# Performance work log

Measured on AMD Instinct MI355X. Metric: run time of the kernel, lower is better.

## Reference

```python
import jax, jax.numpy as jnp
import numpy as np

# ---- MMAL-Net canonical configuration (baked constants of the module) ----
STRIDE = 32          # backbone stride: feature cell -> input pixels
FM = 14              # feature-map side (448 / 32)
RATIOS = [[4, 4], [3, 5], [5, 3],
          [6, 6], [5, 7], [7, 5],
          [8, 8], [6, 10], [10, 6], [7, 9], [9, 7]]
GROUP_SLICES = [(0, 3), (3, 6), (6, 11)]   # 3 scale groups of ratios
N_LIST = [3, 2, 1]                          # proposals kept per group
IOU_THRESHS = [0.25, 0.25, 0.25]


def _make_coords():
    # pixel-space [x0, y0, x1, y1] per sliding window, row-major (i outer, j inner)
    # matching the row-major flatten of the pooled feature maps.
    c = []
    for rh, rw in RATIOS:
        for i in range(FM - rh + 1):
            for j in range(FM - rw + 1):
                c.append([j * STRIDE, i * STRIDE,
                          (j + rw) * STRIDE - 1, (i + rh) * STRIDE - 1])
    return jnp.asarray(np.array(c, np.float32))

COORDS = _make_coords()                                   # [837, 4]
WIN_NUMS = [(FM - rh + 1) * (FM - rw + 1) for rh, rw in RATIOS]
GROUP_WINS = [sum(WIN_NUMS[a:b]) for a, b in GROUP_SLICES]  # [361, 241, 235]
GROUP_OFFSETS = [0, GROUP_WINS[0], GROUP_WINS[0] + GROUP_WINS[1]]
TOTAL_WINS = sum(GROUP_WINS)                              # 837


def _window_scores(x):
    """sum_c avgpool(x, r) == avgpool(sum_c x, r) -- fuse the channel reduction
    first so we avoid materializing [B, C, h', w'] per ratio."""
    y = jnp.sum(x, axis=1)  # [B, H, W]
    parts = []
    for rh, rw in RATIOS:
        s = jax.lax.reduce_window(y, jnp.float32(0), jax.lax.add,
                                  (1, rh, rw), (1, 1, 1), 'VALID') / (rh * rw)
        parts.append(s.reshape(y.shape[0], -1))
    return jnp.concatenate(parts, axis=1)  # [B, TOTAL_WINS]


def _nms_group(scores, coords, n_sel, iou_thresh):
    """Greedy NMS on one scale group: fixed n_sel iterations of
    (argmax over surviving windows, suppress IoU > thresh). If candidates run
    out, the last selected index is repeated (matches the torch fallback)."""
    W = scores.shape[0]
    area = (coords[:, 2] - coords[:, 0] + 1.) * (coords[:, 3] - coords[:, 1] + 1.)

    def step(carry, _):
        valid, last = carry
        any_v = jnp.any(valid)
        idx = jnp.argmax(jnp.where(valid, scores, -jnp.inf))
        idx = jnp.where(any_v, idx, last)
        sel = coords[idx]
        lt = jnp.maximum(coords[:, :2], sel[:2])
        rb = jnp.minimum(coords[:, 2:], sel[2:])
        wh = rb - lt + 1.
        inter = jnp.where((wh[:, 0] < 0) | (wh[:, 1] < 0), 0., wh[:, 0] * wh[:, 1])
        iou = inter / (area + area[idx] - inter)
        new_valid = (valid & (iou <= iou_thresh)).at[idx].set(False)
        new_valid = jnp.where(any_v, new_valid, valid)
        return (new_valid, idx), idx

    (_, _), sel = jax.lax.scan(step, (jnp.ones(W, bool), jnp.int32(0)),
                               None, length=n_sel)
    return sel  # [n_sel] int32 local indices


def setup_inputs() -> dict:
    key = jax.random.key(0)
    x = jax.random.normal(key, (64, 2048, FM, FM), dtype=jnp.float32)
    return {"x": x, "proposalN": 6}


def reference(x, proposalN):
    all_scores = _window_scores(x)  # [B, 837]
    idx_parts = []
    for g in range(len(N_LIST)):
        off, W = GROUP_OFFSETS[g], GROUP_WINS[g]
        sc = all_scores[:, off:off + W]
        co = COORDS[off:off + W]
        sel = jax.vmap(lambda s: _nms_group(s, co, N_LIST[g], IOU_THRESHS[g]))(sc)
        idx_parts.append(sel + off)
    proposal_indices = jnp.concatenate(idx_parts, axis=1)  # [B, proposalN]
    proposal_scores = jnp.take_along_axis(all_scores, proposal_indices, axis=1)
    return proposal_indices, proposal_scores, all_scores
```

## Files before the change

kernel.cpp:

```cpp
#include <hip/hip_runtime.h>
#include <math.h>

#define B 64
#define C 2048
#define FMH 14
#define HW 196
#define HW4 49
#define CHUNKS 32
#define CPC (C / CHUNKS)
#define NWIN 837
#define KMAX 6

__device__ __constant__ int d_RH[11]   = {4, 3, 5, 6, 5, 7, 8, 6, 10, 7, 9};
__device__ __constant__ int d_RW[11]   = {4, 5, 3, 6, 7, 5, 8, 10, 6, 9, 7};
__device__ __constant__ int d_WOFF[12] = {0, 121, 241, 361, 442, 522, 602, 651, 696, 741, 789, 837};

__global__ __launch_bounds__(256) void sum_channels_kernel(const float4* __restrict__ x,
                                                           float4* __restrict__ partial) {
    const int chunk = blockIdx.x;
    const int b     = blockIdx.y;
    const int lane  = threadIdx.x & 63;
    const int wave  = threadIdx.x >> 6;

    float4 a0 = make_float4(0.f, 0.f, 0.f, 0.f);
    float4 a1 = a0, a2 = a0, a3 = a0;
    if (lane < HW4) {
        const float4* base = x + (size_t)(b * C + chunk * CPC) * HW4 + lane;
        #pragma unroll
        for (int k = 0; k < CPC / 4; k += 4) {
            float4 v0 = base[(size_t)(wave + 4 * (k + 0)) * HW4];
            float4 v1 = base[(size_t)(wave + 4 * (k + 1)) * HW4];
            float4 v2 = base[(size_t)(wave + 4 * (k + 2)) * HW4];
            float4 v3 = base[(size_t)(wave + 4 * (k + 3)) * HW4];
            a0.x += v0.x; a0.y += v0.y; a0.z += v0.z; a0.w += v0.w;
            a1.x += v1.x; a1.y += v1.y; a1.z += v1.z; a1.w += v1.w;
            a2.x += v2.x; a2.y += v2.y; a2.z += v2.z; a2.w += v2.w;
            a3.x += v3.x; a3.y += v3.y; a3.z += v3.z; a3.w += v3.w;
        }
    }
    float4 acc;
    acc.x = (a0.x + a1.x) + (a2.x + a3.x);
    acc.y = (a0.y + a1.y) + (a2.y + a3.y);
    acc.z = (a0.z + a1.z) + (a2.z + a3.z);
    acc.w = (a0.w + a1.w) + (a2.w + a3.w);

    __shared__ float4 sh[256];
    sh[threadIdx.x] = acc;
    __syncthreads();

    if (threadIdx.x < 64 && lane < HW4) {
        float4 c0 = sh[lane], c1 = sh[64 + lane], c2 = sh[128 + lane], c3 = sh[192 + lane];
        float4 s;
        s.x = (c0.x + c1.x) + (c2.x + c3.x);
        s.y = (c0.y + c1.y) + (c2.y + c3.y);
        s.z = (c0.z + c1.z) + (c2.z + c3.z);
        s.w = (c0.w + c1.w) + (c2.w + c3.w);
        partial[(size_t)(b * CHUNKS + chunk) * HW4 + lane] = s;
    }
}

__device__ inline void decode_box(int w, float& x0, float& y0, float& x1, float& y1, float& area) {
    int r = 0;
    while (w >= d_WOFF[r + 1]) ++r;
    int local = w - d_WOFF[r];
    int rh = d_RH[r], rw = d_RW[r];
    int wc = FMH - rw + 1;
    int i = local / wc, j = local - i * wc;
    x0 = (float)(j * 32);
    y0 = (float)(i * 32);
    x1 = (float)((j + rw) * 32 - 1);
    y1 = (float)((i + rh) * 32 - 1);
    area = (float)(rw * 32) * (float)(rh * 32);
}

__global__ __launch_bounds__(256) void scores_nms_kernel(const float* __restrict__ partial,
                                                         float* __restrict__ out) {
    const int g   = blockIdx.x;
    const int b   = blockIdx.y;
    const int tid = threadIdx.x;

    __shared__ float S[15][16];
    __shared__ float sc[361];

    const int ii = tid / FMH, jj = tid % FMH;
    if (tid < HW) {
        const float* p = partial + (size_t)b * CHUNKS * HW + tid;
        float acc = 0.f;
        #pragma unroll
        for (int ch = 0; ch < CHUNKS; ++ch) acc += p[(size_t)ch * HW];
        S[ii + 1][jj + 1] = acc;
    }
    if (tid < 16) S[0][tid] = 0.f;
    if (tid < 15) S[tid][0] = 0.f;
    __syncthreads();

    #pragma unroll
    for (int s = 1; s < 14; s <<= 1) {
        float add = 0.f;
        if (tid < HW && jj >= s) add = S[ii + 1][jj + 1 - s];
        __syncthreads();
        if (tid < HW) S[ii + 1][jj + 1] += add;
        __syncthreads();
    }
    #pragma unroll
    for (int s = 1; s < 14; s <<= 1) {
        float add = 0.f;
        if (tid < HW && ii >= s) add = S[ii + 1 - s][jj + 1];
        __syncthreads();
        if (tid < HW) S[ii + 1][jj + 1] += add;
        __syncthreads();
    }

    const int GOFFc[3] = {0, 361, 602};
    const int GWc[3]   = {361, 241, 235};
    const int NSELc[3] = {3, 2, 1};
    const int SLOTc[3] = {0, 3, 5};
    const int off = GOFFc[g], W = GWc[g];

    for (int wl = tid; wl < W; wl += 256) {
        int w = off + wl;
        int r = 0;
        while (w >= d_WOFF[r + 1]) ++r;
        int local = w - d_WOFF[r];
        int rh = d_RH[r], rw = d_RW[r];
        int wc = FMH - rw + 1;
        int i = local / wc, j = local - i * wc;
        float s = (S[i + rh][j + rw] - S[i][j + rw] - S[i + rh][j] + S[i][j]) / (float)(rh * rw);
        sc[wl] = s;
        out[768 + (size_t)b * NWIN + w] = s;
    }
    __syncthreads();

    if (tid >= 64) return;
    const int lane = tid;

    float sv[KMAX], bx0[KMAX], by0[KMAX], bx1[KMAX], by1[KMAX], bar[KMAX];
    unsigned vmask = 0;
    #pragma unroll
    for (int k = 0; k < KMAX; ++k) {
        int wl = lane + 64 * k;
        if (wl < W) {
            sv[k] = sc[wl];
            decode_box(off + wl, bx0[k], by0[k], bx1[k], by1[k], bar[k]);
            vmask |= (1u << k);
        } else {
            sv[k] = -INFINITY;
        }
    }

    int last = 0;
    const int nsel = NSELc[g];
    for (int it = 0; it < nsel; ++it) {
        float bv = -INFINITY; int bi = 0x7fffffff;
        #pragma unroll
        for (int k = 0; k < KMAX; ++k) {
            if (vmask & (1u << k)) {
                float v = sv[k];
                int wl = lane + 64 * k;
                if (v > bv || (v == bv && wl < bi)) { bv = v; bi = wl; }
            }
        }
        #pragma unroll
        for (int d = 1; d < 64; d <<= 1) {
            float ov = __shfl_xor(bv, d, 64);
            int   oi = __shfl_xor(bi, d, 64);
            if (ov > bv || (ov == bv && oi < bi)) { bv = ov; bi = oi; }
        }
        const bool any = (bv != -INFINITY);
        const int sel = any ? bi : last;
        last = sel;
        if (lane == 0) {
            out[(size_t)b * 6 + SLOTc[g] + it]       = (float)(off + sel);
            out[384 + (size_t)b * 6 + SLOTc[g] + it] = sc[sel];
        }
        if (any) {
            if (it + 1 < nsel) {
                float sx0, sy0, sx1, sy1, sa;
                decode_box(off + sel, sx0, sy0, sx1, sy1, sa);
                #pragma unroll
                for (int k = 0; k < KMAX; ++k) {
                    if (vmask & (1u << k)) {
                        float ltx = fmaxf(bx0[k], sx0), lty = fmaxf(by0[k], sy0);
                        float rbx = fminf(bx1[k], sx1), rby = fminf(by1[k], sy1);
                        float wx = rbx - ltx + 1.f, wy = rby - lty + 1.f;
                        float inter = (wx < 0.f || wy < 0.f) ? 0.f : wx * wy;
                        float iou = inter / (bar[k] + sa - inter);
                        if (iou > 0.25f) vmask &= ~(1u << k);
                    }
                }
            }
            if ((sel & 63) == lane) vmask &= ~(1u << (sel >> 6));
        }
    }
}

extern "C" void kernel_launch(void* const* d_in, const int* in_sizes, int n_in,
                              void* d_out, int out_size, void* d_ws, size_t ws_size,
                              hipStream_t stream) {
    const float* x = (const float*)d_in[0];
    float* out = (float*)d_out;
    float* partial = (float*)d_ws;

    sum_channels_kernel<<<dim3(CHUNKS, B), 256, 0, stream>>>((const float4*)x, (float4*)partial);
    scores_nms_kernel<<<dim3(3, B), 256, 0, stream>>>(partial, out);
}
```

Before: 159.6 us.

## Merge per-group NMS blocks into one block per batch, add nontemporal loads

The score/NMS kernel now launches one block per batch instead of three per batch. The 32-chunk partial reduction and the prefix sum are each done once and shared by all three groups, with one wavefront running NMS per group. The Hillis-Steele integral-image scan with many barriers is replaced by serial row and column scans done by 14 threads. The channel-sum kernel now uses nontemporal vector loads to stream the 100MB input without polluting the cache. The main cost, reading the input, is unchanged, so the second kernel only shaves a few microseconds.

```diff
diff --git a/kernel.cpp b/kernel.cpp
--- a/kernel.cpp
+++ b/kernel.cpp
@@ -11,50 +11,42 @@
 #define NWIN 837
 #define KMAX 6
 
+typedef float f32x4 __attribute__((ext_vector_type(4)));
+
 __device__ __constant__ int d_RH[11]   = {4, 3, 5, 6, 5, 7, 8, 6, 10, 7, 9};
 __device__ __constant__ int d_RW[11]   = {4, 5, 3, 6, 7, 5, 8, 10, 6, 9, 7};
 __device__ __constant__ int d_WOFF[12] = {0, 121, 241, 361, 442, 522, 602, 651, 696, 741, 789, 837};
 
-__global__ __launch_bounds__(256) void sum_channels_kernel(const float4* __restrict__ x,
-                                                           float4* __restrict__ partial) {
+__global__ __launch_bounds__(256) void sum_channels_kernel(const f32x4* __restrict__ x,
+                                                           f32x4* __restrict__ partial) {
     const int chunk = blockIdx.x;
     const int b     = blockIdx.y;
     const int lane  = threadIdx.x & 63;
     const int wave  = threadIdx.x >> 6;
 
-    float4 a0 = make_float4(0.f, 0.f, 0.f, 0.f);
-    float4 a1 = a0, a2 = a0, a3 = a0;
+    f32x4 a0 = (f32x4)(0.f), a1 = (f32x4)(0.f), a2 = (f32x4)(0.f), a3 = (f32x4)(0.f);
     if (lane < HW4) {
-        const float4* base = x + (size_t)(b * C + chunk * CPC) * HW4 + lane;
+        const f32x4* base = x + (size_t)(b * C + chunk * CPC) * HW4 + lane;
         #pragma unroll
         for (int k = 0; k < CPC / 4; k += 4) {
-            float4 v0 = base[(size_t)(wave + 4 * (k + 0)) * HW4];
-            float4 v1 = base[(size_t)(wave + 4 * (k + 1)) * HW4];
-            float4 v2 = base[(size_t)(wave + 4 * (k + 2)) * HW4];
-            float4 v3 = base[(size_t)(wave + 4 * (k + 3)) * HW4];
-            a0.x += v0.x; a0.y += v0.y; a0.z += v0.z; a0.w += v0.w;
-            a1.x += v1.x; a1.y += v1.y; a1.z += v1.z; a1.w += v1.w;
-            a2.x += v2.x; a2.y += v2.y; a2.z += v2.z; a2.w += v2.w;
-            a3.x += v3.x; a3.y += v3.y; a3.z += v3.z; a3.w += v3.w;
+            f32x4 v0 = __builtin_nontemporal_load(&base[(size_t)(wave + 4 * (k + 0)) * HW4]);
+            f32x4 v1 = __builtin_nontemporal_load(&base[(size_t)(wave + 4 * (k + 1)) * HW4]);
+            f32x4 v2 = __builtin_nontemporal_load(&base[(size_t)(wave + 4 * (k + 2)) * HW4]);
+            f32x4 v3 = __builtin_nontemporal_load(&base[(size_t)(wave + 4 * (k + 3)) * HW4]);
+            a0 += v0;
+            a1 += v1;
+            a2 += v2;
+            a3 += v3;
         }
     }
-    float4 acc;
-    acc.x = (a0.x + a1.x) + (a2.x + a3.x);
-    acc.y = (a0.y + a1.y) + (a2.y + a3.y);
-    acc.z = (a0.z + a1.z) + (a2.z + a3.z);
-    acc.w = (a0.w + a1.w) + (a2.w + a3.w);
+    f32x4 acc = (a0 + a1) + (a2 + a3);
 
-    __shared__ float4 sh[256];
+    __shared__ f32x4 sh[256];
     sh[threadIdx.x] = acc;
     __syncthreads();
 
     if (threadIdx.x < 64 && lane < HW4) {
-        float4 c0 = sh[lane], c1 = sh[64 + lane], c2 = sh[128 + lane], c3 = sh[192 + lane];
-        float4 s;
-        s.x = (c0.x + c1.x) + (c2.x + c3.x);
-        s.y = (c0.y + c1.y) + (c2.y + c3.y);
-        s.z = (c0.z + c1.z) + (c2.z + c3.z);
-        s.w = (c0.w + c1.w) + (c2.w + c3.w);
+        f32x4 s = (sh[lane] + sh[64 + lane]) + (sh[128 + lane] + sh[192 + lane]);
         partial[(size_t)(b * CHUNKS + chunk) * HW4 + lane] = s;
     }
 }
@@ -75,41 +67,58 @@
 
 __global__ __launch_bounds__(256) void scores_nms_kernel(const float* __restrict__ partial,
                                                          float* __restrict__ out) {
-    const int g   = blockIdx.x;
-    const int b   = blockIdx.y;
+    const int b   = blockIdx.x;
     const int tid = threadIdx.x;
 
     __shared__ float S[15][16];
-    __shared__ float sc[361];
+    __shared__ float sc[NWIN];
 
-    const int ii = tid / FMH, jj = tid % FMH;
     if (tid < HW) {
         const float* p = partial + (size_t)b * CHUNKS * HW + tid;
         float acc = 0.f;
         #pragma unroll
         for (int ch = 0; ch < CHUNKS; ++ch) acc += p[(size_t)ch * HW];
-        S[ii + 1][jj + 1] = acc;
+        S[tid / FMH + 1][tid % FMH + 1] = acc;
     }
     if (tid < 16) S[0][tid] = 0.f;
     if (tid < 15) S[tid][0] = 0.f;
     __syncthreads();
 
-    #pragma unroll
-    for (int s = 1; s < 14; s <<= 1) {
-        float add = 0.f;
-        if (tid < HW && jj >= s) add = S[ii + 1][jj + 1 - s];
-        __syncthreads();
-        if (tid < HW) S[ii + 1][jj + 1] += add;
-        __syncthreads();
+    if (tid < FMH) {
+        float v[FMH];
+        #pragma unroll
+        for (int j = 0; j < FMH; ++j) v[j] = S[tid + 1][j + 1];
+        float a = 0.f;
+        #pragma unroll
+        for (int j = 0; j < FMH; ++j) { a += v[j]; S[tid + 1][j + 1] = a; }
     }
-    #pragma unroll
-    for (int s = 1; s < 14; s <<= 1) {
-        float add = 0.f;
-        if (tid < HW && ii >= s) add = S[ii + 1 - s][jj + 1];
-        __syncthreads();
-        if (tid < HW) S[ii + 1][jj + 1] += add;
-        __syncthreads();
+    __syncthreads();
+    if (tid < FMH) {
+        float v[FMH];
+        #pragma unroll
+        for (int i = 0; i < FMH; ++i) v[i] = S[i + 1][tid + 1];
+        float a = 0.f;
+        #pragma unroll
+        for (int i = 0; i < FMH; ++i) { a += v[i]; S[i + 1][tid + 1] = a; }
     }
+    __syncthreads();
+
+    for (int w = tid; w < NWIN; w += 256) {
+        int r = 0;
+        while (w >= d_WOFF[r + 1]) ++r;
+        int local = w - d_WOFF[r];
+        int rh = d_RH[r], rw = d_RW[r];
+        int wc = FMH - rw + 1;
+        int i = local / wc, j = local - i * wc;
+        float s = (S[i + rh][j + rw] - S[i][j + rw] - S[i + rh][j] + S[i][j]) / (float)(rh * rw);
+        sc[w] = s;
+        out[768 + (size_t)b * NWIN + w] = s;
+    }
+    __syncthreads();
+
+    const int g = tid >> 6;
+    if (g >= 3) return;
+    const int lane = tid & 63;
 
     const int GOFFc[3] = {0, 361, 602};
     const int GWc[3]   = {361, 241, 235};
@@ -117,30 +126,13 @@
     const int SLOTc[3] = {0, 3, 5};
     const int off = GOFFc[g], W = GWc[g];
 
-    for (int wl = tid; wl < W; wl += 256) {
-        int w = off + wl;
-        int r = 0;
-        while (w >= d_WOFF[r + 1]) ++r;
-        int local = w - d_WOFF[r];
-        int rh = d_RH[r], rw = d_RW[r];
-        int wc = FMH - rw + 1;
-        int i = local / wc, j = local - i * wc;
-        float s = (S[i + rh][j + rw] - S[i][j + rw] - S[i + rh][j] + S[i][j]) / (float)(rh * rw);
-        sc[wl] = s;
-        out[768 + (size_t)b * NWIN + w] = s;
-    }
-    __syncthreads();
-
-    if (tid >= 64) return;
-    const int lane = tid;
-
     float sv[KMAX], bx0[KMAX], by0[KMAX], bx1[KMAX], by1[KMAX], bar[KMAX];
     unsigned vmask = 0;
     #pragma unroll
     for (int k = 0; k < KMAX; ++k) {
         int wl = lane + 64 * k;
         if (wl < W) {
-            sv[k] = sc[wl];
+            sv[k] = sc[off + wl];
             decode_box(off + wl, bx0[k], by0[k], bx1[k], by1[k], bar[k]);
             vmask |= (1u << k);
         } else {
@@ -171,7 +163,7 @@
         last = sel;
         if (lane == 0) {
             out[(size_t)b * 6 + SLOTc[g] + it]       = (float)(off + sel);
-            out[384 + (size_t)b * 6 + SLOTc[g] + it] = sc[sel];
+            out[384 + (size_t)b * 6 + SLOTc[g] + it] = sc[off + sel];
         }
         if (any) {
             if (it + 1 < nsel) {
@@ -201,6 +193,6 @@
     float* out = (float*)d_out;
     float* partial = (float*)d_ws;
 
-    sum_channels_kernel<<<dim3(CHUNKS, B), 256, 0, stream>>>((const float4*)x, (float4*)partial);
-    scores_nms_kernel<<<dim3(3, B), 256, 0, stream>>>(partial, out);
+    sum_channels_kernel<<<dim3(CHUNKS, B), 256, 0, stream>>>((const f32x4*)x, (f32x4*)partial);
+    scores_nms_kernel<<<dim3(B), 256, 0, stream>>>(partial, out);
 }
```

Measured after the change: 148.8 us. 1.07x faster.
